# Kernel tuning notes

Measured on AMD Instinct MI355X. Metric: run time of the kernel, lower is better.

## Reference

```python
import jax, jax.numpy as jnp
import numpy as np
from jax import lax

K = 16
EPS = 1e-5


def setup_inputs() -> dict:
    key = jax.random.key(0)
    k1, k2, k3 = jax.random.split(key, 3)
    x = jax.random.normal(k1, (8, 4096, 64), jnp.float32)
    pos = jax.random.normal(k2, (8, 4096, 3), jnp.float32)
    # nn.Linear(64,128), xavier_uniform weight, zero bias
    limit = float(np.sqrt(6.0 / (64 + 128)))
    W = jax.random.uniform(k3, (128, 64), jnp.float32, -limit, limit)
    b = jnp.zeros((128,), jnp.float32)
    gamma = jnp.ones((128,), jnp.float32)   # BN weight
    beta = jnp.zeros((128,), jnp.float32)   # BN bias
    return {"x": x, "pos": pos, "W": W, "b": b, "gamma": gamma, "beta": beta,
            "n_sampling": 1024}


def _fps(pos3, n_sampling):
    """Farthest point sampling starting at index 0. pos3: [bz,N,3] -> [bz,S] int32."""
    bz, N, _ = pos3.shape

    def step(carry, _):
        min_d, last = carry                                   # [bz,N], [bz]
        lastp = jnp.take_along_axis(pos3, last[:, None, None], axis=1)  # [bz,1,3]
        d = jnp.sum((pos3 - lastp) ** 2, axis=-1)             # [bz,N]
        min_d = jnp.minimum(min_d, d)
        nxt = jnp.argmax(min_d, axis=1).astype(jnp.int32)
        return (min_d, nxt), last

    init = (jnp.full((bz, N), 1e10, pos3.dtype), jnp.zeros((bz,), jnp.int32))
    _, idx = lax.scan(step, init, None, length=n_sampling)    # [S,bz]
    return idx.T                                              # [bz,S]


def _knn_idx(pos3, fps_idx, k):
    """k nearest neighbors (by squared L2) of sampled points among all N points."""
    spos = jnp.take_along_axis(pos3, fps_idx[..., None], axis=1)        # [bz,S,3]
    # ||a-b||^2 = |a|^2 + |b|^2 - 2 a.b, avoids [bz,S,N,3] intermediate
    d = (jnp.sum(spos ** 2, -1)[:, :, None]
         + jnp.sum(pos3 ** 2, -1)[:, None, :]
         - 2.0 * jnp.einsum('bsd,bnd->bsn', spos, pos3))               # [bz,S,N]
    _, idx = lax.top_k(-d, k)                                           # [bz,S,k]
    return idx


def reference(x, pos, W, b, gamma, beta, n_sampling):
    pos3 = pos[..., :3]
    fps_idx = _fps(pos3, n_sampling)                          # [bz,S]
    knn_idx = _knn_idx(pos3, fps_idx, K)                      # [bz,S,K]

    # Linear -> BatchNorm1d (training-mode batch stats, biased var) -> ReLU
    h = jnp.einsum('bnf,of->bno', x, W) + b                   # [bz,N,128]
    mean = h.mean(axis=(0, 1))
    var = h.var(axis=(0, 1))
    h = (h - mean) / jnp.sqrt(var + EPS) * gamma + beta
    h = jax.nn.relu(h)

    # gather k-NN features and max-pool (same math as expand+repeat+gather+max)
    gathered = jax.vmap(lambda hb, ib: hb[ib])(h, knn_idx)    # [bz,S,K,128]
    sampled_knn_x = gathered.max(axis=2)                      # [bz,S,128]

    sampled_pos = jnp.take_along_axis(pos, fps_idx[..., None], axis=1)  # [bz,S,3]
    return sampled_knn_x, sampled_pos
```

## Files before the change

kernel.cpp:

```cpp
#include <hip/hip_runtime.h>
#include <stdint.h>

typedef unsigned long long ull;
typedef float f32x2 __attribute__((ext_vector_type(2)));

#define NBATCH 8
#define NPTS   4096
#define NS     1024
#define NK     16
#define NF     64
#define NO     128

#define FT  256
#define PPT 16

static __device__ __forceinline__ ull umax64(ull a, ull b) { return a > b ? a : b; }
static __device__ __forceinline__ ull umin64(ull a, ull b) { return a < b ? a : b; }

static __device__ __forceinline__ float dist2(const float* plds, int i, float sx,
                                              float sy, float sz) {
  const float dx = plds[i * 3 + 0] - sx;
  const float dy = plds[i * 3 + 1] - sy;
  const float dz = plds[i * 3 + 2] - sz;
  return fmaf(dz, dz, fmaf(dy, dy, dx * dx));
}

static __device__ __forceinline__ ull dpp_min_u64(ull v) {
#define STEP(ctrl)                                                            \
  {                                                                           \
    const unsigned lo = (unsigned)v;                                          \
    const unsigned hi = (unsigned)(v >> 32);                                  \
    const unsigned olo = (unsigned)__builtin_amdgcn_update_dpp(               \
        (int)lo, (int)lo, ctrl, 0xf, 0xf, false);                             \
    const unsigned ohi = (unsigned)__builtin_amdgcn_update_dpp(               \
        (int)hi, (int)hi, ctrl, 0xf, 0xf, false);                             \
    const ull o = ((ull)ohi << 32) | olo;                                     \
    v = o < v ? o : v;                                                        \
  }
  STEP(0x111)
  STEP(0x112)
  STEP(0x114)
  STEP(0x118)
  STEP(0x142)
  STEP(0x143)
#undef STEP
  return v;
}

__global__ __launch_bounds__(256, 1) void fps_stats_kernel(
    const float* __restrict__ pos, const float* __restrict__ x,
    const float* __restrict__ W, const float* __restrict__ bias,
    int* __restrict__ fps_idx, float* __restrict__ out_pos,
    float* __restrict__ partial) {
#pragma clang fp contract(off)
  const int t = threadIdx.x;
  __shared__ float plds[NPTS * 3];
  __shared__ __align__(16) ull wslot[2][4];
  __shared__ int widx_lds[NS];

  if (blockIdx.x >= 8) {
    const int blk = blockIdx.x - 8;
    const int c = t & 127;
    const int h = t >> 7;
    float* xl = plds;

    const float4* Wv = (const float4*)(W + c * NF);
    float4 w[16];
#pragma unroll
    for (int q = 0; q < 16; ++q) w[q] = Wv[q];
    const float bb = bias[c];

    const float4* src = (const float4*)(x + (size_t)blk * 128 * NF);
    float4* dst = (float4*)xl;
    for (int i = t; i < 128 * NF / 4; i += 256) dst[i] = src[i];
    __syncthreads();

    float s = 0.f, s2 = 0.f;
    for (int r = h * 64; r < h * 64 + 64; ++r) {
      const float4* xr = (const float4*)(xl + r * NF);
      float hh = bb;
#pragma unroll
      for (int q = 0; q < 16; ++q) {
        const float4 xv = xr[q];
        hh = fmaf(xv.x, w[q].x, hh);
        hh = fmaf(xv.y, w[q].y, hh);
        hh = fmaf(xv.z, w[q].z, hh);
        hh = fmaf(xv.w, w[q].w, hh);
      }
      s += hh;
      s2 = fmaf(hh, hh, s2);
    }
    partial[(blk * 2 + h) * 256 + c] = s;
    partial[(blk * 2 + h) * 256 + 128 + c] = s2;
    return;
  }

  const int b = blockIdx.x;
  const float* p = pos + (size_t)b * NPTS * 3;
  {
    const float4* src = (const float4*)p;
    float4* dst = (float4*)plds;
    for (int i = t; i < NPTS * 3 / 4; i += FT) dst[i] = src[i];
  }
  if (t == 0) widx_lds[0] = 0;
  __syncthreads();

  f32x2 px2[PPT / 2], py2[PPT / 2], pz2[PPT / 2], md2[PPT / 2];
#pragma unroll
  for (int jp = 0; jp < PPT / 2; ++jp) {
    const int i0 = t + FT * (2 * jp);
    const int i1 = i0 + FT;
    px2[jp] = (f32x2){plds[3 * i0 + 0], plds[3 * i1 + 0]};
    py2[jp] = (f32x2){plds[3 * i0 + 1], plds[3 * i1 + 1]};
    pz2[jp] = (f32x2){plds[3 * i0 + 2], plds[3 * i1 + 2]};
    md2[jp] = (f32x2){1e10f, 1e10f};
  }

  float lx = plds[0], ly = plds[1], lz = plds[2];

  for (int s = 1; s < NS; ++s) {
    const f32x2 lxv = (f32x2){lx, lx};
    const f32x2 lyv = (f32x2){ly, ly};
    const f32x2 lzv = (f32x2){lz, lz};
    f32x2 acc = (f32x2){0.f, 0.f};
#pragma unroll
    for (int jp = 0; jp < PPT / 2; ++jp) {
      const f32x2 dx = px2[jp] - lxv;
      const f32x2 dy = py2[jp] - lyv;
      const f32x2 dz = pz2[jp] - lzv;
      const f32x2 xx = dx * dx;
      const f32x2 yy = dy * dy;
      const f32x2 zz = dz * dz;
      const f32x2 sxy = xx + yy;
      const f32x2 d = sxy + zz;
      md2[jp] = __builtin_elementwise_min(md2[jp], d);
      acc = __builtin_elementwise_max(acc, md2[jp]);
    }
    float best = fmaxf(acc.x, acc.y);
    int lidx = 0;
#pragma unroll
    for (int jp = 0; jp < PPT / 2; ++jp) {
      if (md2[jp].x == best) lidx = t + FT * (2 * jp);
      if (md2[jp].y == best) lidx = t + FT * (2 * jp) + FT;
    }
#define CARRY_STEP(ctrl)                                                     \
    {                                                                        \
      const float bo = __int_as_float(__builtin_amdgcn_update_dpp(           \
          0, __float_as_int(best), ctrl, 0xf, 0xf, true));                   \
      const int io =                                                         \
          __builtin_amdgcn_update_dpp(0, lidx, ctrl, 0xf, 0xf, true);        \
      if (bo > best) {                                                       \
        best = bo;                                                           \
        lidx = io;                                                           \
      }                                                                      \
    }
    CARRY_STEP(0x111)
    CARRY_STEP(0x112)
    CARRY_STEP(0x114)
    CARRY_STEP(0x118)
    CARRY_STEP(0x142)
    CARRY_STEP(0x143)
#undef CARRY_STEP
    if ((t & 63) == 63)
      wslot[s & 1][t >> 6] = ((ull)__float_as_uint(best) << 32) | (unsigned)lidx;
    __syncthreads();
    const ull* wk = wslot[s & 1];
    const ull kk = umax64(umax64(wk[0], wk[1]), umax64(wk[2], wk[3]));
    const int widx = (int)(kk & 0xFFFFFFFFu);
    lx = plds[3 * widx + 0];
    ly = plds[3 * widx + 1];
    lz = plds[3 * widx + 2];
    if (t == 0) widx_lds[s] = widx;
  }

  __syncthreads();
  for (int i = t; i < NS; i += FT) {
    const int wi = widx_lds[i];
    fps_idx[b * NS + i] = wi;
    out_pos[((size_t)b * NS + i) * 3 + 0] = plds[3 * wi + 0];
    out_pos[((size_t)b * NS + i) * 3 + 1] = plds[3 * wi + 1];
    out_pos[((size_t)b * NS + i) * 3 + 2] = plds[3 * wi + 2];
  }
}

__global__ __launch_bounds__(1024) void stats_reduce_kernel(
    const float* __restrict__ partial, const float* __restrict__ gamma,
    const float* __restrict__ beta, float* __restrict__ ab) {
  const int t = threadIdx.x;
  const int c = t & 127;
  const int q = t >> 7;
  __shared__ double sred[1024], s2red[1024];
  double s = 0.0, s2 = 0.0;
#pragma unroll 4
  for (int r = q * 64; r < q * 64 + 64; ++r) {
    s += (double)partial[r * 256 + c];
    s2 += (double)partial[r * 256 + 128 + c];
  }
  sred[t] = s;
  s2red[t] = s2;
  __syncthreads();
  if (t < 128) {
    s = 0.0;
    s2 = 0.0;
#pragma unroll
    for (int qq = 0; qq < 8; ++qq) {
      s += sred[qq * 128 + t];
      s2 += s2red[qq * 128 + t];
    }
    const double n = 32768.0;
    const double mean = s / n;
    const double var = s2 / n - mean * mean;
    const float inv = (float)(1.0 / sqrt(var + 1e-5));
    const float scale = gamma[t] * inv;
    const float shift = beta[t] - (float)mean * scale;
    ab[t] = scale;
    ab[128 + t] = shift;
  }
}

__global__ __launch_bounds__(256, 2) void knn_gather_kernel(
    const float* __restrict__ pos, const int* __restrict__ fps_idx,
    const float* __restrict__ x, const float* __restrict__ W,
    const float* __restrict__ bias, const float* __restrict__ ab,
    float* __restrict__ out) {
  __shared__ float plds[NPTS * 3];
  __shared__ int il2[16 * NK];
  const int b = blockIdx.y;
  const int t = threadIdx.x;
  const int s0 = blockIdx.x * 16;

  {
    const float4* src = (const float4*)(pos + (size_t)b * NPTS * 3);
    float4* dst = (float4*)plds;
    for (int i = t; i < NPTS * 3 / 4; i += 256) dst[i] = src[i];
  }
  __syncthreads();

  const int samp = t >> 4;
  const int chunk = t & 15;
  const int sidx = fps_idx[b * NS + s0 + samp];
  const float sx = plds[sidx * 3 + 0];
  const float sy = plds[sidx * 3 + 1];
  const float sz = plds[sidx * 3 + 2];

  ull k16[16];
#pragma unroll
  for (int k = 0; k < 16; ++k) k16[k] = 0xFFFFFFFF00000000ull | (unsigned)k;
  ull worst = 0xFFFFFFFF0000000Full;
  for (int j = 0; j < 256; ++j) {
    const int i = j * 16 + chunk;
    const float d = dist2(plds, i, sx, sy, sz);
    const ull key = ((ull)__float_as_uint(d) << 32) | (unsigned)i;
    if (key < worst) {
#pragma unroll
      for (int k = 0; k < 16; ++k) k16[k] = (k16[k] == worst) ? key : k16[k];
      ull w01 = umax64(k16[0], k16[1]);
      ull w2 = umax64(umax64(k16[2], k16[3]), umax64(k16[4], k16[5]));
      ull w3 = umax64(umax64(k16[6], k16[7]), umax64(k16[8], k16[9]));
      ull w4 = umax64(umax64(k16[10], k16[11]), umax64(k16[12], k16[13]));
      ull w5 = umax64(k16[14], k16[15]);
      worst = umax64(umax64(w01, w2), umax64(w3, umax64(w4, w5)));
    }
  }
  __syncthreads();
  ull* kbuf = (ull*)plds;
  {
    ull* dst = kbuf + samp * 256 + chunk * 16;
#pragma unroll
    for (int k = 0; k < 16; ++k) dst[k] = k16[k];
  }
  __syncthreads();

  const int wave = t >> 6;
  const int lane = t & 63;
  for (int si = 0; si < 4; ++si) {
    const int s = wave * 4 + si;
    const ull* src = kbuf + s * 256 + lane * 4;
    ull a0 = src[0], a1 = src[1], a2 = src[2], a3 = src[3];
    int kwin = 0;
#pragma unroll
    for (int k = 0; k < 16; ++k) {
      const ull mv = umin64(umin64(a0, a1), umin64(a2, a3));
      const ull wmin = dpp_min_u64(mv);
      const ull win = __shfl(wmin, 63, 64);
      if (lane == k) kwin = (int)(win & 0xFFFFFFFFu);
      a0 = (a0 == win) ? ~0ull : a0;
      a1 = (a1 == win) ? ~0ull : a1;
      a2 = (a2 == win) ? ~0ull : a2;
      a3 = (a3 == win) ? ~0ull : a3;
    }
    if (lane < 16) il2[s * NK + lane] = kwin;
  }

  const int c2 = t & 63;
  const int g = t >> 6;
  float4 w0[16], w1[16];
  {
    const float4* Wv0 = (const float4*)(W + c2 * NF);
    const float4* Wv1 = (const float4*)(W + (c2 + 64) * NF);
#pragma unroll
    for (int q = 0; q < 16; ++q) {
      w0[q] = Wv0[q];
      w1[q] = Wv1[q];
    }
  }
  const float bb0 = bias[c2], bb1 = bias[c2 + 64];
  const float scale0 = ab[c2], scale1 = ab[c2 + 64];
  const float shift0 = ab[128 + c2], shift1 = ab[128 + c2 + 64];
  const float* xb = x + (size_t)b * NPTS * NF;
  float* xtile = plds;

  for (int pass = 0; pass < 4; ++pass) {
    __syncthreads();
    {
      const int r = t & 63;
      const int q0 = (t >> 6) * 4;
      const int idx = il2[(pass * 4 + (r >> 4)) * NK + (r & 15)];
      const float4* srow = (const float4*)(xb + (size_t)idx * NF);
      float4* drow = (float4*)(xtile + r * NF);
#pragma unroll
      for (int q = q0; q < q0 + 4; ++q) drow[q] = srow[q];
    }
    __syncthreads();

    float m0 = 0.0f, m1 = 0.0f;
#pragma unroll
    for (int k = 0; k < NK; ++k) {
      const float4* xr = (const float4*)(xtile + (g * 16 + k) * NF);
      float h0 = bb0, h1 = bb1;
#pragma unroll
      for (int q = 0; q < 16; ++q) {
        const float4 xv = xr[q];
        h0 = fmaf(xv.x, w0[q].x, h0);
        h0 = fmaf(xv.y, w0[q].y, h0);
        h0 = fmaf(xv.z, w0[q].z, h0);
        h0 = fmaf(xv.w, w0[q].w, h0);
        h1 = fmaf(xv.x, w1[q].x, h1);
        h1 = fmaf(xv.y, w1[q].y, h1);
        h1 = fmaf(xv.z, w1[q].z, h1);
        h1 = fmaf(xv.w, w1[q].w, h1);
      }
      h0 = fmaf(h0, scale0, shift0);
      h1 = fmaf(h1, scale1, shift1);
      h0 = h0 > 0.f ? h0 : 0.f;
      h1 = h1 > 0.f ? h1 : 0.f;
      m0 = m0 > h0 ? m0 : h0;
      m1 = m1 > h1 ? m1 : h1;
    }
    float* o = out + ((size_t)b * NS + s0 + pass * 4 + g) * NO;
    o[c2] = m0;
    o[c2 + 64] = m1;
  }
}

extern "C" void kernel_launch(void* const* d_in, const int* in_sizes, int n_in,
                              void* d_out, int out_size, void* d_ws, size_t ws_size,
                              hipStream_t stream) {
  const float* x     = (const float*)d_in[0];
  const float* pos   = (const float*)d_in[1];
  const float* W     = (const float*)d_in[2];
  const float* bias  = (const float*)d_in[3];
  const float* gamma = (const float*)d_in[4];
  const float* beta  = (const float*)d_in[5];

  float* out_knn = (float*)d_out;
  float* out_pos = out_knn + (size_t)NBATCH * NS * NO;

  char* ws = (char*)d_ws;
  int* fps_idx   = (int*)(ws);
  float* partial = (float*)(ws + (32 << 10));
  float* ab      = (float*)(ws + (544 << 10));

  fps_stats_kernel<<<8 + 256, 256, 0, stream>>>(pos, x, W, bias, fps_idx,
                                                out_pos, partial);
  stats_reduce_kernel<<<1, 1024, 0, stream>>>(partial, gamma, beta, ab);
  knn_gather_kernel<<<dim3(64, NBATCH), 256, 0, stream>>>(pos, fps_idx, x, W,
                                                          bias, ab, out_knn);
}
```

Measured before the change: 943.8 us.

## Fuse FPS, BN stats and kNN gather into one persistent kernel with progress flags

Merges the three launches into one kernel. The 8 FPS blocks publish sampled indices in chunks of 64 through atomic progress counters, so the kNN/gather blocks can start as soon as their 32 samples exist. Those blocks also compute the BN partial statistics, and block 0 reduces them behind a completion flag. The aim is to overlap the serial FPS with kNN and gather work and to drop launch gaps. The cost is spin-wait synchronisation that assumes all 264 blocks are resident at once, plus an extra memset.

```diff
diff --git a/kernel.cpp b/kernel.cpp
--- a/kernel.cpp
+++ b/kernel.cpp
@@ -47,30 +47,158 @@
   return v;
 }
 
-__global__ __launch_bounds__(256, 1) void fps_stats_kernel(
+static __device__ __forceinline__ void spin_ge(int* p, int v) {
+  int it = 0;
+  while (__hip_atomic_load(p, __ATOMIC_ACQUIRE, __HIP_MEMORY_SCOPE_AGENT) < v) {
+    __builtin_amdgcn_s_sleep(8);
+    if (++it > 100000000) break;
+  }
+}
+
+__global__ __launch_bounds__(256) void mega_kernel(
     const float* __restrict__ pos, const float* __restrict__ x,
     const float* __restrict__ W, const float* __restrict__ bias,
+    const float* __restrict__ gamma, const float* __restrict__ beta,
     int* __restrict__ fps_idx, float* __restrict__ out_pos,
-    float* __restrict__ partial) {
+    float* __restrict__ partial, float* __restrict__ ab,
+    int* __restrict__ flags, float* __restrict__ out) {
 #pragma clang fp contract(off)
   const int t = threadIdx.x;
   __shared__ float plds[NPTS * 3];
   __shared__ __align__(16) ull wslot[2][4];
   __shared__ int widx_lds[NS];
-
-  if (blockIdx.x >= 8) {
-    const int blk = blockIdx.x - 8;
+  __shared__ int il2[32 * NK];
+  __shared__ double dred[512];
+
+  int* progress = flags;
+  int* stats_done = flags + 8;
+  int* ab_flag = flags + 9;
+
+  if (blockIdx.x < 8) {
+    const int b = blockIdx.x;
+    {
+      const float4* src = (const float4*)(pos + (size_t)b * NPTS * 3);
+      float4* dst = (float4*)plds;
+      for (int i = t; i < NPTS * 3 / 4; i += FT) dst[i] = src[i];
+    }
+    if (t == 0) widx_lds[0] = 0;
+    __syncthreads();
+
+    f32x2 px2[PPT / 2], py2[PPT / 2], pz2[PPT / 2], md2[PPT / 2];
+#pragma unroll
+    for (int jp = 0; jp < PPT / 2; ++jp) {
+      const int i0 = t + FT * (2 * jp);
+      const int i1 = i0 + FT;
+      px2[jp] = (f32x2){plds[3 * i0 + 0], plds[3 * i1 + 0]};
+      py2[jp] = (f32x2){plds[3 * i0 + 1], plds[3 * i1 + 1]};
+      pz2[jp] = (f32x2){plds[3 * i0 + 2], plds[3 * i1 + 2]};
+      md2[jp] = (f32x2){1e10f, 1e10f};
+    }
+
+    float lx = plds[0], ly = plds[1], lz = plds[2];
+
+    for (int s = 1; s < NS; ++s) {
+      const f32x2 lxv = (f32x2){lx, lx};
+      const f32x2 lyv = (f32x2){ly, ly};
+      const f32x2 lzv = (f32x2){lz, lz};
+      f32x2 acc = (f32x2){0.f, 0.f};
+#pragma unroll
+      for (int jp = 0; jp < PPT / 2; ++jp) {
+        const f32x2 dx = px2[jp] - lxv;
+        const f32x2 dy = py2[jp] - lyv;
+        const f32x2 dz = pz2[jp] - lzv;
+        const f32x2 xx = dx * dx;
+        const f32x2 yy = dy * dy;
+        const f32x2 zz = dz * dz;
+        const f32x2 sxy = xx + yy;
+        const f32x2 d = sxy + zz;
+        md2[jp] = __builtin_elementwise_min(md2[jp], d);
+        acc = __builtin_elementwise_max(acc, md2[jp]);
+      }
+      float best = fmaxf(acc.x, acc.y);
+      int lidx = 0;
+#pragma unroll
+      for (int jp = 0; jp < PPT / 2; ++jp) {
+        if (md2[jp].x == best) lidx = t + FT * (2 * jp);
+        if (md2[jp].y == best) lidx = t + FT * (2 * jp) + FT;
+      }
+#define CARRY_STEP(ctrl)                                                     \
+      {                                                                      \
+        const float bo = __int_as_float(__builtin_amdgcn_update_dpp(         \
+            0, __float_as_int(best), ctrl, 0xf, 0xf, true));                 \
+        const int io =                                                       \
+            __builtin_amdgcn_update_dpp(0, lidx, ctrl, 0xf, 0xf, true);      \
+        if (bo > best) {                                                     \
+          best = bo;                                                         \
+          lidx = io;                                                         \
+        }                                                                    \
+      }
+      CARRY_STEP(0x111)
+      CARRY_STEP(0x112)
+      CARRY_STEP(0x114)
+      CARRY_STEP(0x118)
+      CARRY_STEP(0x142)
+      CARRY_STEP(0x143)
+#undef CARRY_STEP
+      if ((t & 63) == 63)
+        wslot[s & 1][t >> 6] =
+            ((ull)__float_as_uint(best) << 32) | (unsigned)lidx;
+      __syncthreads();
+
+      if ((s & 63) == 0) {
+        if (t < 64)
+          __hip_atomic_store(&fps_idx[b * NS + (s - 64) + t],
+                             widx_lds[(s - 64) + t], __ATOMIC_RELAXED,
+                             __HIP_MEMORY_SCOPE_AGENT);
+        __threadfence();
+        __syncthreads();
+        if (t == 0)
+          __hip_atomic_store(&progress[b], s, __ATOMIC_RELEASE,
+                             __HIP_MEMORY_SCOPE_AGENT);
+      }
+
+      const ull* wk = wslot[s & 1];
+      const ull kk = umax64(umax64(wk[0], wk[1]), umax64(wk[2], wk[3]));
+      const int widx = (int)(kk & 0xFFFFFFFFu);
+      lx = plds[3 * widx + 0];
+      ly = plds[3 * widx + 1];
+      lz = plds[3 * widx + 2];
+      if (t == 0) widx_lds[s] = widx;
+    }
+
+    __syncthreads();
+    for (int i = t; i < NS; i += FT) {
+      const int wi = widx_lds[i];
+      out_pos[((size_t)b * NS + i) * 3 + 0] = plds[3 * wi + 0];
+      out_pos[((size_t)b * NS + i) * 3 + 1] = plds[3 * wi + 1];
+      out_pos[((size_t)b * NS + i) * 3 + 2] = plds[3 * wi + 2];
+    }
+    if (t < 64)
+      __hip_atomic_store(&fps_idx[b * NS + 960 + t], widx_lds[960 + t],
+                         __ATOMIC_RELAXED, __HIP_MEMORY_SCOPE_AGENT);
+    __threadfence();
+    __syncthreads();
+    if (t == 0)
+      __hip_atomic_store(&progress[b], NS, __ATOMIC_RELEASE,
+                         __HIP_MEMORY_SCOPE_AGENT);
+    return;
+  }
+
+  const int w = blockIdx.x - 8;
+  const int b = w >> 5;
+  const int s0 = (w & 31) * 32;
+
+  {
     const int c = t & 127;
     const int h = t >> 7;
     float* xl = plds;
-
     const float4* Wv = (const float4*)(W + c * NF);
-    float4 w[16];
-#pragma unroll
-    for (int q = 0; q < 16; ++q) w[q] = Wv[q];
+    float4 wreg[16];
+#pragma unroll
+    for (int q = 0; q < 16; ++q) wreg[q] = Wv[q];
     const float bb = bias[c];
 
-    const float4* src = (const float4*)(x + (size_t)blk * 128 * NF);
+    const float4* src = (const float4*)(x + (size_t)w * 128 * NF);
     float4* dst = (float4*)xl;
     for (int i = t; i < 128 * NF / 4; i += 256) dst[i] = src[i];
     __syncthreads();
@@ -82,162 +210,67 @@
 #pragma unroll
       for (int q = 0; q < 16; ++q) {
         const float4 xv = xr[q];
-        hh = fmaf(xv.x, w[q].x, hh);
-        hh = fmaf(xv.y, w[q].y, hh);
-        hh = fmaf(xv.z, w[q].z, hh);
-        hh = fmaf(xv.w, w[q].w, hh);
+        hh = fmaf(xv.x, wreg[q].x, hh);
+        hh = fmaf(xv.y, wreg[q].y, hh);
+        hh = fmaf(xv.z, wreg[q].z, hh);
+        hh = fmaf(xv.w, wreg[q].w, hh);
       }
       s += hh;
       s2 = fmaf(hh, hh, s2);
     }
-    partial[(blk * 2 + h) * 256 + c] = s;
-    partial[(blk * 2 + h) * 256 + 128 + c] = s2;
-    return;
-  }
-
-  const int b = blockIdx.x;
-  const float* p = pos + (size_t)b * NPTS * 3;
-  {
-    const float4* src = (const float4*)p;
-    float4* dst = (float4*)plds;
-    for (int i = t; i < NPTS * 3 / 4; i += FT) dst[i] = src[i];
-  }
-  if (t == 0) widx_lds[0] = 0;
-  __syncthreads();
-
-  f32x2 px2[PPT / 2], py2[PPT / 2], pz2[PPT / 2], md2[PPT / 2];
-#pragma unroll
-  for (int jp = 0; jp < PPT / 2; ++jp) {
-    const int i0 = t + FT * (2 * jp);
-    const int i1 = i0 + FT;
-    px2[jp] = (f32x2){plds[3 * i0 + 0], plds[3 * i1 + 0]};
-    py2[jp] = (f32x2){plds[3 * i0 + 1], plds[3 * i1 + 1]};
-    pz2[jp] = (f32x2){plds[3 * i0 + 2], plds[3 * i1 + 2]};
-    md2[jp] = (f32x2){1e10f, 1e10f};
-  }
-
-  float lx = plds[0], ly = plds[1], lz = plds[2];
-
-  for (int s = 1; s < NS; ++s) {
-    const f32x2 lxv = (f32x2){lx, lx};
-    const f32x2 lyv = (f32x2){ly, ly};
-    const f32x2 lzv = (f32x2){lz, lz};
-    f32x2 acc = (f32x2){0.f, 0.f};
-#pragma unroll
-    for (int jp = 0; jp < PPT / 2; ++jp) {
-      const f32x2 dx = px2[jp] - lxv;
-      const f32x2 dy = py2[jp] - lyv;
-      const f32x2 dz = pz2[jp] - lzv;
-      const f32x2 xx = dx * dx;
-      const f32x2 yy = dy * dy;
-      const f32x2 zz = dz * dz;
-      const f32x2 sxy = xx + yy;
-      const f32x2 d = sxy + zz;
-      md2[jp] = __builtin_elementwise_min(md2[jp], d);
-      acc = __builtin_elementwise_max(acc, md2[jp]);
-    }
-    float best = fmaxf(acc.x, acc.y);
-    int lidx = 0;
-#pragma unroll
-    for (int jp = 0; jp < PPT / 2; ++jp) {
-      if (md2[jp].x == best) lidx = t + FT * (2 * jp);
-      if (md2[jp].y == best) lidx = t + FT * (2 * jp) + FT;
-    }
-#define CARRY_STEP(ctrl)                                                     \
-    {                                                                        \
-      const float bo = __int_as_float(__builtin_amdgcn_update_dpp(           \
-          0, __float_as_int(best), ctrl, 0xf, 0xf, true));                   \
-      const int io =                                                         \
-          __builtin_amdgcn_update_dpp(0, lidx, ctrl, 0xf, 0xf, true);        \
-      if (bo > best) {                                                       \
-        best = bo;                                                           \
-        lidx = io;                                                           \
-      }                                                                      \
-    }
-    CARRY_STEP(0x111)
-    CARRY_STEP(0x112)
-    CARRY_STEP(0x114)
-    CARRY_STEP(0x118)
-    CARRY_STEP(0x142)
-    CARRY_STEP(0x143)
-#undef CARRY_STEP
-    if ((t & 63) == 63)
-      wslot[s & 1][t >> 6] = ((ull)__float_as_uint(best) << 32) | (unsigned)lidx;
-    __syncthreads();
-    const ull* wk = wslot[s & 1];
-    const ull kk = umax64(umax64(wk[0], wk[1]), umax64(wk[2], wk[3]));
-    const int widx = (int)(kk & 0xFFFFFFFFu);
-    lx = plds[3 * widx + 0];
-    ly = plds[3 * widx + 1];
-    lz = plds[3 * widx + 2];
-    if (t == 0) widx_lds[s] = widx;
-  }
-
-  __syncthreads();
-  for (int i = t; i < NS; i += FT) {
-    const int wi = widx_lds[i];
-    fps_idx[b * NS + i] = wi;
-    out_pos[((size_t)b * NS + i) * 3 + 0] = plds[3 * wi + 0];
-    out_pos[((size_t)b * NS + i) * 3 + 1] = plds[3 * wi + 1];
-    out_pos[((size_t)b * NS + i) * 3 + 2] = plds[3 * wi + 2];
-  }
-}
-
-__global__ __launch_bounds__(1024) void stats_reduce_kernel(
-    const float* __restrict__ partial, const float* __restrict__ gamma,
-    const float* __restrict__ beta, float* __restrict__ ab) {
-  const int t = threadIdx.x;
-  const int c = t & 127;
-  const int q = t >> 7;
-  __shared__ double sred[1024], s2red[1024];
-  double s = 0.0, s2 = 0.0;
+    partial[(w * 2 + h) * 256 + c] = s;
+    partial[(w * 2 + h) * 256 + 128 + c] = s2;
+    __threadfence();
+    __syncthreads();
+    if (t == 0)
+      __hip_atomic_fetch_add(stats_done, 1, __ATOMIC_RELEASE,
+                             __HIP_MEMORY_SCOPE_AGENT);
+  }
+
+  if (w == 0) {
+    if (t == 0) spin_ge(stats_done, 256);
+    __syncthreads();
+    const int c = t & 127;
+    const int q = t >> 7;
+    double s = 0.0, s2 = 0.0;
 #pragma unroll 4
-  for (int r = q * 64; r < q * 64 + 64; ++r) {
-    s += (double)partial[r * 256 + c];
-    s2 += (double)partial[r * 256 + 128 + c];
-  }
-  sred[t] = s;
-  s2red[t] = s2;
-  __syncthreads();
-  if (t < 128) {
-    s = 0.0;
-    s2 = 0.0;
-#pragma unroll
-    for (int qq = 0; qq < 8; ++qq) {
-      s += sred[qq * 128 + t];
-      s2 += s2red[qq * 128 + t];
-    }
-    const double n = 32768.0;
-    const double mean = s / n;
-    const double var = s2 / n - mean * mean;
-    const float inv = (float)(1.0 / sqrt(var + 1e-5));
-    const float scale = gamma[t] * inv;
-    const float shift = beta[t] - (float)mean * scale;
-    ab[t] = scale;
-    ab[128 + t] = shift;
-  }
-}
-
-__global__ __launch_bounds__(256, 2) void knn_gather_kernel(
-    const float* __restrict__ pos, const int* __restrict__ fps_idx,
-    const float* __restrict__ x, const float* __restrict__ W,
-    const float* __restrict__ bias, const float* __restrict__ ab,
-    float* __restrict__ out) {
-  __shared__ float plds[NPTS * 3];
-  __shared__ int il2[16 * NK];
-  const int b = blockIdx.y;
-  const int t = threadIdx.x;
-  const int s0 = blockIdx.x * 16;
-
+    for (int r = q * 256; r < q * 256 + 256; ++r) {
+      s += (double)partial[r * 256 + c];
+      s2 += (double)partial[r * 256 + 128 + c];
+    }
+    dred[t] = s;
+    dred[256 + t] = s2;
+    __syncthreads();
+    if (t < 128) {
+      s = dred[t] + dred[t + 128];
+      s2 = dred[256 + t] + dred[256 + t + 128];
+      const double n = 32768.0;
+      const double mean = s / n;
+      const double var = s2 / n - mean * mean;
+      const float inv = (float)(1.0 / sqrt(var + 1e-5));
+      const float scale = gamma[t] * inv;
+      const float shift = beta[t] - (float)mean * scale;
+      ab[t] = scale;
+      ab[128 + t] = shift;
+    }
+    __threadfence();
+    __syncthreads();
+    if (t == 0)
+      __hip_atomic_store(ab_flag, 1, __ATOMIC_RELEASE,
+                         __HIP_MEMORY_SCOPE_AGENT);
+  }
+
+  __syncthreads();
   {
     const float4* src = (const float4*)(pos + (size_t)b * NPTS * 3);
     float4* dst = (float4*)plds;
     for (int i = t; i < NPTS * 3 / 4; i += 256) dst[i] = src[i];
   }
-  __syncthreads();
-
-  const int samp = t >> 4;
-  const int chunk = t & 15;
+  if (t == 0) spin_ge(&progress[b], s0 + 32);
+  __syncthreads();
+
+  const int samp = t >> 3;
+  const int chunk = t & 7;
   const int sidx = fps_idx[b * NS + s0 + samp];
   const float sx = plds[sidx * 3 + 0];
   const float sy = plds[sidx * 3 + 1];
@@ -247,8 +280,8 @@
 #pragma unroll
   for (int k = 0; k < 16; ++k) k16[k] = 0xFFFFFFFF00000000ull | (unsigned)k;
   ull worst = 0xFFFFFFFF0000000Full;
-  for (int j = 0; j < 256; ++j) {
-    const int i = j * 16 + chunk;
+  for (int j = 0; j < 512; ++j) {
+    const int i = j * 8 + chunk;
     const float d = dist2(plds, i, sx, sy, sz);
     const ull key = ((ull)__float_as_uint(d) << 32) | (unsigned)i;
     if (key < worst) {
@@ -265,32 +298,34 @@
   __syncthreads();
   ull* kbuf = (ull*)plds;
   {
-    ull* dst = kbuf + samp * 256 + chunk * 16;
+    ull* dst = kbuf + samp * 128 + chunk * 16;
 #pragma unroll
     for (int k = 0; k < 16; ++k) dst[k] = k16[k];
   }
   __syncthreads();
 
-  const int wave = t >> 6;
+  const int wv = t >> 6;
   const int lane = t & 63;
-  for (int si = 0; si < 4; ++si) {
-    const int s = wave * 4 + si;
-    const ull* src = kbuf + s * 256 + lane * 4;
-    ull a0 = src[0], a1 = src[1], a2 = src[2], a3 = src[3];
+  for (int si = 0; si < 8; ++si) {
+    const int s = wv * 8 + si;
+    const ull* src = kbuf + s * 128 + lane * 2;
+    ull a0 = src[0], a1 = src[1];
     int kwin = 0;
 #pragma unroll
     for (int k = 0; k < 16; ++k) {
-      const ull mv = umin64(umin64(a0, a1), umin64(a2, a3));
+      const ull mv = umin64(a0, a1);
       const ull wmin = dpp_min_u64(mv);
       const ull win = __shfl(wmin, 63, 64);
       if (lane == k) kwin = (int)(win & 0xFFFFFFFFu);
       a0 = (a0 == win) ? ~0ull : a0;
       a1 = (a1 == win) ? ~0ull : a1;
-      a2 = (a2 == win) ? ~0ull : a2;
-      a3 = (a3 == win) ? ~0ull : a3;
     }
     if (lane < 16) il2[s * NK + lane] = kwin;
   }
+  __syncthreads();
+
+  if (w != 0 && t == 0) spin_ge(ab_flag, 1);
+  __syncthreads();
 
   const int c2 = t & 63;
   const int g = t >> 6;
@@ -310,8 +345,7 @@
   const float* xb = x + (size_t)b * NPTS * NF;
   float* xtile = plds;
 
-  for (int pass = 0; pass < 4; ++pass) {
-    __syncthreads();
+  for (int pass = 0; pass < 8; ++pass) {
     {
       const int r = t & 63;
       const int q0 = (t >> 6) * 4;
@@ -350,6 +384,7 @@
     float* o = out + ((size_t)b * NS + s0 + pass * 4 + g) * NO;
     o[c2] = m0;
     o[c2 + 64] = m1;
+    __syncthreads();
   }
 }
 
@@ -370,10 +405,10 @@
   int* fps_idx   = (int*)(ws);
   float* partial = (float*)(ws + (32 << 10));
   float* ab      = (float*)(ws + (544 << 10));
-
-  fps_stats_kernel<<<8 + 256, 256, 0, stream>>>(pos, x, W, bias, fps_idx,
-                                                out_pos, partial);
-  stats_reduce_kernel<<<1, 1024, 0, stream>>>(partial, gamma, beta, ab);
-  knn_gather_kernel<<<dim3(64, NBATCH), 256, 0, stream>>>(pos, fps_idx, x, W,
-                                                          bias, ab, out_knn);
+  int* flags     = (int*)(ws + (560 << 10));
+
+  hipMemsetAsync(flags, 0, 64, stream);
+  mega_kernel<<<8 + 256, 256, 0, stream>>>(pos, x, W, bias, gamma, beta,
+                                           fps_idx, out_pos, partial, ab,
+                                           flags, out_knn);
 }
```

Result: slower. 1.201 ms (+27.3%).
